# Kernel optimization log

Measured on AMD Instinct MI355X. Metric: run time of the kernel, lower is better.

The kernel has to match this reference:

```python
import jax, jax.numpy as jnp
import numpy as np

WS = 7          # window size
NH = 12         # num heads
DIM = 384
HD = DIM // NH  # head dim = 32
EPS = 1e-5


def _ln(x, g, b):
    m = x.mean(-1, keepdims=True)
    v = ((x - m) ** 2).mean(-1, keepdims=True)
    return (x - m) / jnp.sqrt(v + EPS) * g + b


def _rel_index():
    # exact replica of WindowAttention.__init__ relative_position_index
    coords = np.stack(np.meshgrid(np.arange(WS), np.arange(WS), indexing='ij'))  # (2,ws,ws)
    flat = coords.reshape(2, -1)                                                 # (2,49)
    rel = flat[:, :, None] - flat[:, None, :]                                    # (2,49,49)
    rel = rel.transpose(1, 2, 0).astype(np.int32)
    rel[:, :, 0] += WS - 1
    rel[:, :, 1] += WS - 1
    rel[:, :, 0] *= 2 * WS - 1
    return jnp.asarray(rel.sum(-1))  # (49,49), values in [0, 169)


def setup_inputs() -> dict:
    key = jax.random.key(0)
    ks = jax.random.split(key, 16)
    B, H, W = 16, 56, 56
    L = H * W
    hidden = int(DIM * 4.0)
    p = lambda k, shp: (jax.random.normal(k, shp, jnp.float32) * 0.02)
    return {
        'x': jax.random.normal(ks[0], (B, L, DIM), jnp.float32),
        'kv': jax.random.normal(ks[1], (2, B, NH, WS * WS, HD), jnp.float32),
        'rel_index': _rel_index(),
        'H': H, 'W': W,
        'g1': jnp.ones((DIM,), jnp.float32), 'b1': jnp.zeros((DIM,), jnp.float32),
        'Wqkv': p(ks[2], (DIM, 3 * DIM)), 'bqkv': jnp.zeros((3 * DIM,), jnp.float32),
        'bias_table': p(ks[3], ((2 * WS - 1) ** 2, NH)),
        'Wproj': p(ks[4], (DIM, DIM)), 'bproj': jnp.zeros((DIM,), jnp.float32),
        'g2': jnp.ones((DIM,), jnp.float32), 'b2': jnp.zeros((DIM,), jnp.float32),
        'Wfc1': p(ks[5], (DIM, hidden)), 'bfc1': jnp.zeros((hidden,), jnp.float32),
        'Wfc2': p(ks[6], (hidden, DIM)), 'bfc2': jnp.zeros((DIM,), jnp.float32),
    }


def reference(x, kv, rel_index, H, W, g1, b1, Wqkv, bqkv, bias_table, Wproj, bproj,
              g2, b2, Wfc1, bfc1, Wfc2, bfc2):
    B, L, C = x.shape
    scale = HD ** -0.5
    nWh, nWw = H // WS, W // WS  # H,W divisible by WS -> pad is a no-op; shift_size=0 -> no roll/mask

    h = _ln(x, g1, b1).reshape(B, H, W, C)
    # window_partition -> (B*nW, N, C), N = WS*WS
    hw = h.reshape(B, nWh, WS, nWw, WS, C).transpose(0, 1, 3, 2, 4, 5).reshape(-1, WS * WS, C)
    B_, N, _ = hw.shape

    qkv = (hw @ Wqkv + bqkv).reshape(B_, N, 3, NH, HD).transpose(2, 0, 3, 1, 4)  # (3,B_,nh,N,hd)
    q = qkv[0] * scale
    k, v = kv[0], kv[1]                     # (B, nh, num_kv, hd)
    reps = B_ // k.shape[0]
    k = jnp.repeat(k, reps, axis=0)         # repeat_interleave: each image's windows share its kv
    v = jnp.repeat(v, reps, axis=0)

    attn = jnp.einsum('bhqd,bhkd->bhqk', q, k)                      # (B_,nh,N,N)
    bias = bias_table[rel_index.reshape(-1)].reshape(N, N, NH).transpose(2, 0, 1)
    attn = jax.nn.softmax(attn + bias[None], axis=-1)
    o = jnp.einsum('bhqk,bhkd->bhqd', attn, v)                      # (B_,nh,N,hd)
    o = o.transpose(0, 2, 1, 3).reshape(B_, N, C) @ Wproj + bproj

    # window_reverse -> (B, L, C)
    o = o.reshape(B, nWh, nWw, WS, WS, C).transpose(0, 1, 3, 2, 4, 5).reshape(B, L, C)
    x = x + o
    x = x + (jax.nn.gelu(_ln(x, g2, b2) @ Wfc1 + bfc1, approximate=False) @ Wfc2 + bfc2)
    return x
```

## Files before the change

### kernel.cpp

```cpp
#include <hip/hip_runtime.h>

typedef __attribute__((ext_vector_type(8))) short short8;
typedef __attribute__((ext_vector_type(4))) float floatx4;
typedef unsigned int u32;

#define DIM 384
#define NHEAD 12
#define HDIM 32

__device__ __forceinline__ float bf2f(unsigned int u) {
    union { unsigned int i; float f; } x; x.i = (u & 0xffffu) << 16; return x.f;
}
__device__ __forceinline__ unsigned short f2bf(float f) {
    union { float f; unsigned int i; } x; x.f = f;
    return (unsigned short)((x.i + 0x7fffu + ((x.i >> 16) & 1u)) >> 16);
}

__device__ __forceinline__ int nat2win(int r) {
    int b = r / 3136; int l = r - b * 3136;
    int hh = l / 56, wc = l - hh * 56;
    int wh = hh / 7, nr = hh - wh * 7;
    int ww = wc / 7, nc = wc - ww * 7;
    return ((b << 6) + wh * 8 + ww) * 49 + nr * 7 + nc;
}
__device__ __forceinline__ int win2nat(int r) {
    int w = r / 49; int n = r - w * 49;
    int b = w >> 6; int wi = w & 63;
    int wh = wi >> 3, ww = wi & 7;
    int hh = wh * 7 + n / 7, wc = ww * 7 + n % 7;
    return b * 3136 + hh * 56 + wc;
}

#define GLOAD_LDS16(g, l) \
    __builtin_amdgcn_global_load_lds((const __attribute__((address_space(1))) u32*)(g), \
                                     (__attribute__((address_space(3))) u32*)(l), 16, 0, 0)

__global__ void transpose_kernel(const float* __restrict__ src,
                                 unsigned short* __restrict__ dst,
                                 int K, int N, int ld) {
    int i = blockIdx.x * blockDim.x + threadIdx.x;
    if (i >= K * N) return;
    int n = i / K, k = i - n * K;
    dst[i] = f2bf(src[(size_t)k * ld + n]);
}

__global__ void bias_expand_kernel(const int* __restrict__ rel_index,
                                   const float* __restrict__ bias_table,
                                   float* __restrict__ biasx) {
    int i = blockIdx.x * blockDim.x + threadIdx.x;
    if (i >= NHEAD * 49 * 49) return;
    int h = i / 2401, r = i - h * 2401;
    biasx[i] = bias_table[rel_index[r] * NHEAD + h];
}

__global__ __launch_bounds__(64) void ln_kernel(const float* __restrict__ x,
                                                const float* __restrict__ g,
                                                const float* __restrict__ b,
                                                unsigned short* __restrict__ out,
                                                int windowed) {
    int r = blockIdx.x;
    int lane = threadIdx.x;
    const float* row = x + (size_t)r * DIM;
    float v[6];
    float s = 0.f, ss = 0.f;
#pragma unroll
    for (int j = 0; j < 3; j++) {
        int c = lane + j * 64;
        float2 f = *(const float2*)(row + 2 * c);
        v[2 * j] = f.x; v[2 * j + 1] = f.y;
        s += f.x + f.y; ss += f.x * f.x + f.y * f.y;
    }
#pragma unroll
    for (int m = 1; m < 64; m <<= 1) {
        s += __shfl_xor(s, m);
        ss += __shfl_xor(ss, m);
    }
    float mean = s * (1.f / DIM);
    float var = ss * (1.f / DIM) - mean * mean;
    float rstd = rsqrtf(var + 1e-5f);
    int orow = windowed ? nat2win(r) : r;
    unsigned short* op = out + (size_t)orow * DIM;
#pragma unroll
    for (int j = 0; j < 3; j++) {
        int c = lane + j * 64;
        float2 gg = *(const float2*)(g + 2 * c);
        float2 bb = *(const float2*)(b + 2 * c);
        float o0 = (v[2 * j] - mean) * rstd * gg.x + bb.x;
        float o1 = (v[2 * j + 1] - mean) * rstd * gg.y + bb.y;
        unsigned int w = ((unsigned int)f2bf(o1) << 16) | f2bf(o0);
        *(unsigned int*)(op + 2 * c) = w;
    }
}

__global__ __launch_bounds__(256) void attn_kernel(const unsigned short* __restrict__ q,
                                                   const float* __restrict__ kv,
                                                   const float* __restrict__ biasx,
                                                   unsigned short* __restrict__ o) {
    __shared__ alignas(16) unsigned short Ks[64 * 40];
    __shared__ alignas(16) unsigned short Vt[32 * 72];
    __shared__ float Bi[49 * 52];
    __shared__ alignas(16) unsigned short Ps[4][16 * 72];

    int blk = blockIdx.x;
    int b = blk / 48; int rem = blk - b * 48;
    int h = rem >> 2; int g = rem & 3;
    size_t row_base = (size_t)(b * 64 + g * 16) * 49;

    int t = threadIdx.x;
    int lane = t & 63;
    int wv = t >> 6;
    int lr = lane & 15;
    int lg = lane >> 4;

    const float* kptr = kv + (size_t)(b * NHEAD + h) * 1568;
    for (int idx = t; idx < 392; idx += 256) {
        int row = idx >> 3, seg = idx & 7;
        float4 f = *(const float4*)(kptr + row * 32 + seg * 4);
        ushort4 h4; h4.x = f2bf(f.x); h4.y = f2bf(f.y); h4.z = f2bf(f.z); h4.w = f2bf(f.w);
        *(ushort4*)&Ks[row * 40 + seg * 4] = h4;
    }
    const float* vptr = kv + (size_t)(192 + b * NHEAD + h) * 1568;
    for (int idx = t; idx < 784; idx += 256) {
        int m = idx >> 4, dp = idx & 15;
        float2 f = *(const float2*)(vptr + m * 32 + dp * 2);
        Vt[(2 * dp) * 72 + m]     = f2bf(f.x);
        Vt[(2 * dp + 1) * 72 + m] = f2bf(f.y);
    }
    for (int idx = t; idx < 32 * 23; idx += 256) {
        int d = idx / 23, m = 49 + idx - d * 23;
        Vt[d * 72 + m] = 0;
    }
    const float* bh = biasx + h * 2401;
    for (int idx = t; idx < 2401; idx += 256) {
        int qr = idx / 49, k = idx - qr * 49;
        Bi[qr * 52 + k] = bh[idx];
    }
    __syncthreads();

    short8 bfr[4], vbf[2][2];
#pragma unroll
    for (int ni = 0; ni < 4; ni++)
        bfr[ni] = *(const short8*)&Ks[(ni * 16 + lr) * 40 + lg * 8];
#pragma unroll
    for (int ni = 0; ni < 2; ni++)
#pragma unroll
        for (int ks = 0; ks < 2; ks++)
            vbf[ni][ks] = *(const short8*)&Vt[(ni * 16 + lr) * 72 + ks * 32 + lg * 8];

    const unsigned short* qb = q + row_base * DIM + h * 32 + lg * 8;
    unsigned short* ob = o + row_base * DIM + h * 32;

    short8 af = *(const short8*)(qb + (size_t)(wv * 16 + lr) * DIM);
    for (int tm = wv; tm < 49; tm += 4) {
        short8 af_next;
        if (tm + 4 < 49) af_next = *(const short8*)(qb + (size_t)((tm + 4) * 16 + lr) * DIM);

        floatx4 sfrag[4];
#pragma unroll
        for (int ni = 0; ni < 4; ni++)
            sfrag[ni] = __builtin_amdgcn_mfma_f32_16x16x32_bf16(af, bfr[ni], (floatx4)0.f, 0, 0, 0);

#pragma unroll
        for (int reg = 0; reg < 4; reg++) {
            int r_loc = tm * 16 + lg * 4 + reg;
            int qr = r_loc % 49;
            float mx = -1e30f;
#pragma unroll
            for (int ni = 0; ni < 4; ni++) {
                int k = ni * 16 + lr;
                float s = sfrag[ni][reg];
                if (k < 49) s += Bi[qr * 52 + k];
                else s = -1e30f;
                sfrag[ni][reg] = s;
                mx = fmaxf(mx, s);
            }
#pragma unroll
            for (int j = 1; j < 16; j <<= 1) mx = fmaxf(mx, __shfl_xor(mx, j));
            float sum = 0.f;
#pragma unroll
            for (int ni = 0; ni < 4; ni++) {
                float e = __expf(sfrag[ni][reg] - mx);
                sfrag[ni][reg] = e;
                sum += e;
            }
#pragma unroll
            for (int j = 1; j < 16; j <<= 1) sum += __shfl_xor(sum, j);
            float inv = 1.f / sum;
#pragma unroll
            for (int ni = 0; ni < 4; ni++)
                Ps[wv][(lg * 4 + reg) * 72 + ni * 16 + lr] = f2bf(sfrag[ni][reg] * inv);
        }
        floatx4 ofrag[2] = {(floatx4)0.f, (floatx4)0.f};
#pragma unroll
        for (int ks = 0; ks < 2; ks++) {
            short8 paf = *(const short8*)&Ps[wv][lr * 72 + ks * 32 + lg * 8];
#pragma unroll
            for (int ni = 0; ni < 2; ni++)
                ofrag[ni] = __builtin_amdgcn_mfma_f32_16x16x32_bf16(paf, vbf[ni][ks], ofrag[ni], 0, 0, 0);
        }
#pragma unroll
        for (int reg = 0; reg < 4; reg++) {
            size_t rg = (size_t)(tm * 16 + lg * 4 + reg) * DIM;
#pragma unroll
            for (int ni = 0; ni < 2; ni++)
                ob[rg + ni * 16 + lr] = f2bf(ofrag[ni][reg]);
        }
        af = af_next;
    }
}

template <int DO_GELU, int DO_REMAP, int OUT_BF16>
__global__ __launch_bounds__(256) void gemm_kernel(const unsigned short* __restrict__ A,
                                                   const unsigned short* __restrict__ Bt,
                                                   const float* __restrict__ bias,
                                                   const float* __restrict__ res,
                                                   void* __restrict__ outv,
                                                   int M, int N, int K, float scale) {
    __shared__ alignas(16) unsigned short As[2][128 * 64];
    __shared__ alignas(16) unsigned short Bs[2][128 * 64];
    int m0 = blockIdx.y * 128;
    int n0 = blockIdx.x * 128;
    int t = threadIdx.x;
    int lane = t & 63;
    int wv = t >> 6;
    int wm = (wv >> 1) * 64, wn = (wv & 1) * 64;
    int lr = lane & 15;
    int lq = lane >> 4;

    int rowB = t >> 3;
    int colOff = (((t & 7) ^ ((t >> 3) & 7)) << 3);
    int sw0 = ((lq ^ (lr & 7)) << 3);
    int sw1 = (((4 + lq) ^ (lr & 7)) << 3);

    floatx4 acc[4][4];
#pragma unroll
    for (int i = 0; i < 4; i++)
#pragma unroll
        for (int j = 0; j < 4; j++) acc[i][j] = (floatx4)0.f;

    auto stage = [&](int buf, int kk) {
#pragma unroll
        for (int i = 0; i < 4; i++) {
            int row = i * 32 + rowB;
            GLOAD_LDS16(A + (size_t)(m0 + row) * K + kk + colOff, &As[buf][(i * 256 + t) * 8]);
            GLOAD_LDS16(Bt + (size_t)(n0 + row) * K + kk + colOff, &Bs[buf][(i * 256 + t) * 8]);
        }
    };

    const int nk = K >> 6;
    stage(0, 0);
    stage(1, 64);

    for (int kt = 0; kt < nk; ++kt) {
        int cur = kt & 1;
        if (kt + 1 < nk) asm volatile("s_waitcnt vmcnt(8)" ::: "memory");
        else             asm volatile("s_waitcnt vmcnt(0)" ::: "memory");
        __builtin_amdgcn_s_barrier();
        asm volatile("" ::: "memory");
#pragma unroll
        for (int ksub = 0; ksub < 2; ksub++) {
            int sw = ksub ? sw1 : sw0;
            short8 af[4], bfr[4];
#pragma unroll
            for (int i = 0; i < 4; i++) {
                af[i] = *(const short8*)(&As[cur][(wm + i * 16 + lr) * 64 + sw]);
                bfr[i] = *(const short8*)(&Bs[cur][(wn + i * 16 + lr) * 64 + sw]);
            }
#pragma unroll
            for (int i = 0; i < 4; i++)
#pragma unroll
                for (int j = 0; j < 4; j++)
                    acc[i][j] = __builtin_amdgcn_mfma_f32_16x16x32_bf16(af[i], bfr[j], acc[i][j], 0, 0, 0);
        }
        __builtin_amdgcn_s_barrier();
        asm volatile("" ::: "memory");
        if (kt + 2 < nk) stage(cur, (kt + 2) << 6);
    }

#pragma unroll
    for (int j = 0; j < 4; j++) {
        int gcol = n0 + wn + j * 16 + lr;
        float bv = bias[gcol];
#pragma unroll
        for (int i = 0; i < 4; i++) {
#pragma unroll
            for (int r = 0; r < 4; r++) {
                int grow = m0 + wm + i * 16 + lq * 4 + r;
                float val = acc[i][j][r] + bv;
                if (DO_GELU) val = 0.5f * val * (1.f + erff(val * 0.70710678118654752f));
                val *= scale;
                int orow = DO_REMAP ? win2nat(grow) : grow;
                size_t idx = (size_t)orow * N + gcol;
                if (res) val += res[idx];
                if (OUT_BF16) ((unsigned short*)outv)[idx] = f2bf(val);
                else          ((float*)outv)[idx] = val;
            }
        }
    }
}

extern "C" void kernel_launch(void* const* d_in, const int* in_sizes, int n_in,
                              void* d_out, int out_size, void* d_ws, size_t ws_size,
                              hipStream_t stream) {
    const float* x          = (const float*)d_in[0];
    const float* kv         = (const float*)d_in[1];
    const int*   rel_index  = (const int*)d_in[2];
    const float* g1         = (const float*)d_in[5];
    const float* b1         = (const float*)d_in[6];
    const float* Wqkv       = (const float*)d_in[7];
    const float* bqkv       = (const float*)d_in[8];
    const float* bias_table = (const float*)d_in[9];
    const float* Wproj      = (const float*)d_in[10];
    const float* bproj      = (const float*)d_in[11];
    const float* g2         = (const float*)d_in[12];
    const float* b2         = (const float*)d_in[13];
    const float* Wfc1       = (const float*)d_in[14];
    const float* bfc1       = (const float*)d_in[15];
    const float* Wfc2       = (const float*)d_in[16];
    const float* bfc2       = (const float*)d_in[17];
    float* out = (float*)d_out;

    char* ws = (char*)d_ws;
    unsigned short* wq_t   = (unsigned short*)(ws);
    unsigned short* wp_t   = (unsigned short*)(ws + 294912);
    unsigned short* wfc1_t = (unsigned short*)(ws + 589824);
    unsigned short* wfc2_t = (unsigned short*)(ws + 1769472);
    float*          biasx  = (float*)(ws + 2949120);
    unsigned short* bufA   = (unsigned short*)(ws + 3080192);
    unsigned short* bufB   = (unsigned short*)(ws + 3080192 + 38535168);

    const int M = 50176;
    const float scale = 0.17677669529663687f;
    const int full_mlp = (ws_size >= (size_t)3080192 + 38535168 + 154140672);

    transpose_kernel<<<(384 * 384 + 255) / 256, 256, 0, stream>>>(Wqkv, wq_t, 384, 384, 1152);
    transpose_kernel<<<(384 * 384 + 255) / 256, 256, 0, stream>>>(Wproj, wp_t, 384, 384, 384);
    transpose_kernel<<<(384 * 1536 + 255) / 256, 256, 0, stream>>>(Wfc1, wfc1_t, 384, 1536, 1536);
    transpose_kernel<<<(1536 * 384 + 255) / 256, 256, 0, stream>>>(Wfc2, wfc2_t, 1536, 384, 384);
    bias_expand_kernel<<<(NHEAD * 2401 + 255) / 256, 256, 0, stream>>>(rel_index, bias_table, biasx);

    ln_kernel<<<M, 64, 0, stream>>>(x, g1, b1, bufA, 1);
    gemm_kernel<0, 0, 1><<<dim3(3, 392), 256, 0, stream>>>(bufA, wq_t, bqkv, nullptr, bufB,
                                                           M, 384, 384, scale);
    attn_kernel<<<16 * NHEAD * 4, 256, 0, stream>>>(bufB, kv, biasx, bufA);
    gemm_kernel<0, 1, 0><<<dim3(3, 392), 256, 0, stream>>>(bufA, wp_t, bproj, x, d_out,
                                                           M, 384, 384, 1.f);
    ln_kernel<<<M, 64, 0, stream>>>(out, g2, b2, bufA, 0);

    if (full_mlp) {
        gemm_kernel<1, 0, 1><<<dim3(12, 392), 256, 0, stream>>>(bufA, wfc1_t, bfc1,
                                                                nullptr, bufB, M, 1536, 384, 1.f);
        gemm_kernel<0, 0, 0><<<dim3(3, 392), 256, 0, stream>>>(bufB, wfc2_t, bfc2,
                                                               out, out, M, 384, 1536, 1.f);
    } else {
        for (int c = 0; c < 4; c++) {
            size_t ro = (size_t)c * 12544;
            gemm_kernel<1, 0, 1><<<dim3(12, 98), 256, 0, stream>>>(bufA + ro * 384, wfc1_t, bfc1,
                                                                   nullptr, bufB, 12544, 1536, 384, 1.f);
            gemm_kernel<0, 0, 0><<<dim3(3, 98), 256, 0, stream>>>(bufB, wfc2_t, bfc2,
                                                                  out + ro * 384, out + ro * 384,
                                                                  12544, 384, 1536, 1.f);
        }
    }
}
```

Before: 678.2 us.

## Fuse MLP fc1+GELU+fc2 into one kernel keeping hidden activations on-chip

Replaces the two separate MLP GEMM launches (fc1 with GELU writing a large bf16 hidden buffer, then fc2 reading it back) with a single fused kernel. Each 64-row block computes 128-column hidden chunks with MFMA, applies bias and GELU, stages them in LDS per wave, and accumulates the fc2 output in 24 register accumulators. This removes the global round-trip of the 50176x1536 hidden tensor. In exchange, weights are read directly from global memory without LDS tiling or reuse across waves, and register pressure is high, which may limit occupancy.

```diff
diff --git a/kernel.cpp b/kernel.cpp
--- a/kernel.cpp
+++ b/kernel.cpp
@@ -295,6 +295,80 @@
                 if (OUT_BF16) ((unsigned short*)outv)[idx] = f2bf(val);
                 else          ((float*)outv)[idx] = val;
             }
+        }
+    }
+}
+
+__global__ __launch_bounds__(256, 2) void fused_mlp_kernel(
+    const unsigned short* __restrict__ A,
+    const unsigned short* __restrict__ W1t,
+    const unsigned short* __restrict__ W2t,
+    const float* __restrict__ b1,
+    const float* __restrict__ b2,
+    float* __restrict__ io) {
+    __shared__ alignas(16) unsigned short hl[4][16 * 136];
+
+    int t = threadIdx.x;
+    int lane = t & 63;
+    int wv = t >> 6;
+    int lr = lane & 15;
+    int lg = lane >> 4;
+    int r0 = blockIdx.x * 64 + wv * 16;
+
+    const unsigned short* arow = A + (size_t)(r0 + lr) * 384 + lg * 8;
+    unsigned short* hw = &hl[wv][0];
+
+    floatx4 oacc[24];
+#pragma unroll
+    for (int j = 0; j < 24; j++) oacc[j] = (floatx4)0.f;
+
+    for (int c = 0; c < 12; c++) {
+        __syncthreads();
+
+        floatx4 S[8];
+#pragma unroll
+        for (int n = 0; n < 8; n++) S[n] = (floatx4)0.f;
+        const unsigned short* w1 = W1t + (size_t)(c * 128 + lr) * 384 + lg * 8;
+#pragma unroll
+        for (int k = 0; k < 12; k++) {
+            short8 af = *(const short8*)(arow + k * 32);
+#pragma unroll
+            for (int n = 0; n < 8; n++) {
+                short8 bf = *(const short8*)(w1 + (size_t)(n * 16) * 384 + k * 32);
+                S[n] = __builtin_amdgcn_mfma_f32_16x16x32_bf16(af, bf, S[n], 0, 0, 0);
+            }
+        }
+
+#pragma unroll
+        for (int n = 0; n < 8; n++) {
+            float bb = b1[c * 128 + n * 16 + lr];
+#pragma unroll
+            for (int reg = 0; reg < 4; reg++) {
+                float v = S[n][reg] + bb;
+                v = 0.5f * v * (1.f + erff(v * 0.70710678118654752f));
+                hw[(lg * 4 + reg) * 136 + n * 16 + lr] = f2bf(v);
+            }
+        }
+
+        const unsigned short* w2 = W2t + (size_t)lr * 1536 + c * 128 + lg * 8;
+#pragma unroll
+        for (int k2 = 0; k2 < 4; k2++) {
+            short8 paf = *(const short8*)&hw[lr * 136 + k2 * 32 + lg * 8];
+#pragma unroll
+            for (int n2 = 0; n2 < 24; n2++) {
+                short8 bf2 = *(const short8*)(w2 + (size_t)(n2 * 16) * 1536 + k2 * 32);
+                oacc[n2] = __builtin_amdgcn_mfma_f32_16x16x32_bf16(paf, bf2, oacc[n2], 0, 0, 0);
+            }
+        }
+    }
+
+#pragma unroll
+    for (int n2 = 0; n2 < 24; n2++) {
+        float bb = b2[n2 * 16 + lr];
+#pragma unroll
+        for (int reg = 0; reg < 4; reg++) {
+            size_t idx = (size_t)(r0 + lg * 4 + reg) * 384 + n2 * 16 + lr;
+            io[idx] = io[idx] + oacc[n2][reg] + bb;
         }
     }
 }
@@ -331,7 +405,6 @@
 
     const int M = 50176;
     const float scale = 0.17677669529663687f;
-    const int full_mlp = (ws_size >= (size_t)3080192 + 38535168 + 154140672);
 
     transpose_kernel<<<(384 * 384 + 255) / 256, 256, 0, stream>>>(Wqkv, wq_t, 384, 384, 1152);
     transpose_kernel<<<(384 * 384 + 255) / 256, 256, 0, stream>>>(Wproj, wp_t, 384, 384, 384);
@@ -346,20 +419,7 @@
     gemm_kernel<0, 1, 0><<<dim3(3, 392), 256, 0, stream>>>(bufA, wp_t, bproj, x, d_out,
                                                            M, 384, 384, 1.f);
     ln_kernel<<<M, 64, 0, stream>>>(out, g2, b2, bufA, 0);
-
-    if (full_mlp) {
-        gemm_kernel<1, 0, 1><<<dim3(12, 392), 256, 0, stream>>>(bufA, wfc1_t, bfc1,
-                                                                nullptr, bufB, M, 1536, 384, 1.f);
-        gemm_kernel<0, 0, 0><<<dim3(3, 392), 256, 0, stream>>>(bufB, wfc2_t, bfc2,
-                                                               out, out, M, 384, 1536, 1.f);
-    } else {
-        for (int c = 0; c < 4; c++) {
-            size_t ro = (size_t)c * 12544;
-            gemm_kernel<1, 0, 1><<<dim3(12, 98), 256, 0, stream>>>(bufA + ro * 384, wfc1_t, bfc1,
-                                                                   nullptr, bufB, 12544, 1536, 384, 1.f);
-            gemm_kernel<0, 0, 0><<<dim3(3, 98), 256, 0, stream>>>(bufB, wfc2_t, bfc2,
-                                                                  out + ro * 384, out + ro * 384,
-                                                                  12544, 384, 1536, 1.f);
-        }
-    }
-}
+    fused_mlp_kernel<<<M / 64, 256, 0, stream>>>(bufA, wfc1_t, wfc2_t, bfc1, bfc2, out);
+
+    (void)bufB; (void)ws_size;
+}
```

New measurement: 1.430 ms. 2.11x slower.

## Remap GEMM workgroups across XCDs and stage A through registers

Applied to the files above, without the earlier changes.

Remaps the linear workgroup id so that each XCD gets a contiguous range of output tiles, which is meant to improve L2 locality across the eight XCDs. It also changes the A-operand path from direct global-to-LDS loads to register-staged loads that are prefetched one extra k-step ahead, while B keeps the direct LDS path. The vmcnt waits are restructured to match the new load ordering. This adds register pressure and extra waits in the mainloop, and a wrong vmcnt count could expose stale data.

```diff
diff --git a/kernel.cpp b/kernel.cpp
--- a/kernel.cpp
+++ b/kernel.cpp
@@ -218,8 +218,15 @@
                                                    int M, int N, int K, float scale) {
     __shared__ alignas(16) unsigned short As[2][128 * 64];
     __shared__ alignas(16) unsigned short Bs[2][128 * 64];
-    int m0 = blockIdx.y * 128;
-    int n0 = blockIdx.x * 128;
+
+    int nwg = gridDim.x * gridDim.y;
+    int lid = blockIdx.y * gridDim.x + blockIdx.x;
+    int q8 = nwg >> 3, r8 = nwg & 7;
+    int xcd = lid & 7, pos = lid >> 3;
+    int nlid = (xcd < r8 ? xcd * (q8 + 1) : r8 * (q8 + 1) + (xcd - r8) * q8) + pos;
+    int m0 = (nlid / gridDim.x) * 128;
+    int n0 = (nlid % gridDim.x) * 128;
+
     int t = threadIdx.x;
     int lane = t & 63;
     int wv = t >> 6;
@@ -238,23 +245,45 @@
 #pragma unroll
         for (int j = 0; j < 4; j++) acc[i][j] = (floatx4)0.f;
 
-    auto stage = [&](int buf, int kk) {
-#pragma unroll
-        for (int i = 0; i < 4; i++) {
-            int row = i * 32 + rowB;
-            GLOAD_LDS16(A + (size_t)(m0 + row) * K + kk + colOff, &As[buf][(i * 256 + t) * 8]);
-            GLOAD_LDS16(Bt + (size_t)(n0 + row) * K + kk + colOff, &Bs[buf][(i * 256 + t) * 8]);
-        }
+    short8 ar[4];
+    const unsigned short* Abase = A + (size_t)(m0 + rowB) * K + colOff;
+    const unsigned short* Bbase = Bt + (size_t)(n0 + rowB) * K + colOff;
+    size_t rstep = (size_t)32 * K;
+
+    auto loadA = [&](int kk) {
+#pragma unroll
+        for (int i = 0; i < 4; i++)
+            ar[i] = *(const short8*)(Abase + (size_t)i * rstep + kk);
     };
+    auto writeA = [&](int buf) {
+#pragma unroll
+        for (int i = 0; i < 4; i++)
+            *(short8*)&As[buf][(i * 256 + t) * 8] = ar[i];
+    };
+    auto gloadB = [&](int buf, int kk) {
+#pragma unroll
+        for (int i = 0; i < 4; i++)
+            GLOAD_LDS16(Bbase + (size_t)i * rstep + kk, &Bs[buf][(i * 256 + t) * 8]);
+    };
 
     const int nk = K >> 6;
-    stage(0, 0);
-    stage(1, 64);
+
+    loadA(0);
+    gloadB(0, 0);
+    asm volatile("s_waitcnt vmcnt(4)" ::: "memory");
+    writeA(0);
+    loadA(64);
+    gloadB(1, 64);
+    asm volatile("s_waitcnt vmcnt(4)" ::: "memory");
+    writeA(1);
+    if (nk > 2) loadA(128);
+    asm volatile("s_waitcnt lgkmcnt(0)" ::: "memory");
 
     for (int kt = 0; kt < nk; ++kt) {
         int cur = kt & 1;
-        if (kt + 1 < nk) asm volatile("s_waitcnt vmcnt(8)" ::: "memory");
-        else             asm volatile("s_waitcnt vmcnt(0)" ::: "memory");
+        if (kt + 2 < nk)      asm volatile("s_waitcnt vmcnt(8)" ::: "memory");
+        else if (kt + 1 < nk) asm volatile("s_waitcnt vmcnt(4)" ::: "memory");
+        else                  asm volatile("s_waitcnt vmcnt(0)" ::: "memory");
         __builtin_amdgcn_s_barrier();
         asm volatile("" ::: "memory");
 #pragma unroll
@@ -274,7 +303,13 @@
         }
         __builtin_amdgcn_s_barrier();
         asm volatile("" ::: "memory");
-        if (kt + 2 < nk) stage(cur, (kt + 2) << 6);
+        if (kt + 2 < nk) {
+            gloadB(cur, (kt + 2) << 6);
+            asm volatile("s_waitcnt vmcnt(4)" ::: "memory");
+            writeA(cur);
+            if (kt + 3 < nk) loadA((kt + 3) << 6);
+            asm volatile("s_waitcnt lgkmcnt(0)" ::: "memory");
+        }
     }
 
 #pragma unroll
```

Result: faster. 658.0 us (-3.0%).

## Restructure GEMM to 128x384 tiles with register-resident A fragments

Applied to the files above, without the earlier changes.

The GEMM kernel now uses 512-thread blocks that each compute a 128-row by 384-column strip. Only the weight (B) tile is staged in LDS (double-buffered, 96 KB). A fragments are loaded straight from global memory into registers and prefetched one k-step ahead. The goal is to read each A row once per 384 output columns instead of once per 128, and to cut the number of blocks and LDS traffic for A. The cost is far higher LDS use and register pressure (96 accumulator registers per thread), which limits occupancy, and A loads become uncached strided per-lane global reads.

```diff
diff --git a/kernel.cpp b/kernel.cpp
--- a/kernel.cpp
+++ b/kernel.cpp
@@ -210,87 +210,123 @@
 }
 
 template <int DO_GELU, int DO_REMAP, int OUT_BF16>
-__global__ __launch_bounds__(256) void gemm_kernel(const unsigned short* __restrict__ A,
-                                                   const unsigned short* __restrict__ Bt,
-                                                   const float* __restrict__ bias,
-                                                   const float* __restrict__ res,
-                                                   void* __restrict__ outv,
-                                                   int M, int N, int K, float scale) {
-    __shared__ alignas(16) unsigned short As[2][128 * 64];
-    __shared__ alignas(16) unsigned short Bs[2][128 * 64];
+__global__ __launch_bounds__(512, 3) void gemm_kernel(const unsigned short* __restrict__ A,
+                                                      const unsigned short* __restrict__ Bt,
+                                                      const float* __restrict__ bias,
+                                                      const float* __restrict__ res,
+                                                      void* __restrict__ outv,
+                                                      int Nstride, int K, float scale) {
+    __shared__ alignas(16) unsigned short Bs[2][384 * 64];
+
+    int chunk = blockIdx.x;
     int m0 = blockIdx.y * 128;
-    int n0 = blockIdx.x * 128;
+    const unsigned short* Bc = Bt + (size_t)chunk * 384 * K;
+    int colbase = chunk * 384;
+
     int t = threadIdx.x;
     int lane = t & 63;
     int wv = t >> 6;
-    int wm = (wv >> 1) * 64, wn = (wv & 1) * 64;
+    int wm = (wv >> 1) * 32;
+    int wn2 = (wv & 1) * 192;
     int lr = lane & 15;
     int lq = lane >> 4;
 
-    int rowB = t >> 3;
-    int colOff = (((t & 7) ^ ((t >> 3) & 7)) << 3);
+    int colOffB = (((t & 7) ^ ((t >> 3) & 7)) << 3);
     int sw0 = ((lq ^ (lr & 7)) << 3);
     int sw1 = (((4 + lq) ^ (lr & 7)) << 3);
 
-    floatx4 acc[4][4];
-#pragma unroll
-    for (int i = 0; i < 4; i++)
-#pragma unroll
-        for (int j = 0; j < 4; j++) acc[i][j] = (floatx4)0.f;
-
-    auto stage = [&](int buf, int kk) {
-#pragma unroll
-        for (int i = 0; i < 4; i++) {
-            int row = i * 32 + rowB;
-            GLOAD_LDS16(A + (size_t)(m0 + row) * K + kk + colOff, &As[buf][(i * 256 + t) * 8]);
-            GLOAD_LDS16(Bt + (size_t)(n0 + row) * K + kk + colOff, &Bs[buf][(i * 256 + t) * 8]);
+    floatx4 acc[2][12];
+#pragma unroll
+    for (int m = 0; m < 2; m++)
+#pragma unroll
+        for (int n2 = 0; n2 < 12; n2++) acc[m][n2] = (floatx4)0.f;
+
+    const unsigned short* Arow0 = A + (size_t)(m0 + wm + lr) * K + lq * 8;
+    const unsigned short* Arow1 = A + (size_t)(m0 + wm + 16 + lr) * K + lq * 8;
+
+    auto gloadB = [&](int buf, int kk) {
+#pragma unroll
+        for (int i = 0; i < 6; i++) {
+            int slot = i * 512 + t;
+            int row = slot >> 3;
+            GLOAD_LDS16(Bc + (size_t)row * K + kk + colOffB, &Bs[buf][slot * 8]);
         }
     };
 
     const int nk = K >> 6;
-    stage(0, 0);
-    stage(1, 64);
-
-    for (int kt = 0; kt < nk; ++kt) {
-        int cur = kt & 1;
-        if (kt + 1 < nk) asm volatile("s_waitcnt vmcnt(8)" ::: "memory");
-        else             asm volatile("s_waitcnt vmcnt(0)" ::: "memory");
-        __builtin_amdgcn_s_barrier();
-        asm volatile("" ::: "memory");
-#pragma unroll
-        for (int ksub = 0; ksub < 2; ksub++) {
-            int sw = ksub ? sw1 : sw0;
-            short8 af[4], bfr[4];
-#pragma unroll
-            for (int i = 0; i < 4; i++) {
-                af[i] = *(const short8*)(&As[cur][(wm + i * 16 + lr) * 64 + sw]);
-                bfr[i] = *(const short8*)(&Bs[cur][(wn + i * 16 + lr) * 64 + sw]);
+
+    short8 aX00, aX01, aX10, aX11, aY00, aY01, aY10, aY11;
+
+    gloadB(0, 0);
+    aX00 = *(const short8*)(Arow0);
+    aX01 = *(const short8*)(Arow0 + 32);
+    aX10 = *(const short8*)(Arow1);
+    aX11 = *(const short8*)(Arow1 + 32);
+    gloadB(1, 64);
+
+    auto compute = [&](int buf, const short8& a00, const short8& a01,
+                       const short8& a10, const short8& a11) {
+#pragma unroll
+        for (int n2 = 0; n2 < 12; n2++) {
+            int r = wn2 + n2 * 16 + lr;
+            short8 bf0 = *(const short8*)&Bs[buf][r * 64 + sw0];
+            short8 bf1 = *(const short8*)&Bs[buf][r * 64 + sw1];
+            acc[0][n2] = __builtin_amdgcn_mfma_f32_16x16x32_bf16(a00, bf0, acc[0][n2], 0, 0, 0);
+            acc[1][n2] = __builtin_amdgcn_mfma_f32_16x16x32_bf16(a10, bf0, acc[1][n2], 0, 0, 0);
+            acc[0][n2] = __builtin_amdgcn_mfma_f32_16x16x32_bf16(a01, bf1, acc[0][n2], 0, 0, 0);
+            acc[1][n2] = __builtin_amdgcn_mfma_f32_16x16x32_bf16(a11, bf1, acc[1][n2], 0, 0, 0);
+        }
+    };
+
+    for (int kt = 0; kt < nk; kt += 2) {
+        {
+            int kk1 = (kt + 1) << 6;
+            aY00 = *(const short8*)(Arow0 + kk1);
+            aY01 = *(const short8*)(Arow0 + kk1 + 32);
+            aY10 = *(const short8*)(Arow1 + kk1);
+            aY11 = *(const short8*)(Arow1 + kk1 + 32);
+            asm volatile("s_waitcnt vmcnt(10)" ::: "memory");
+            __builtin_amdgcn_s_barrier();
+            asm volatile("" ::: "memory");
+            compute(0, aX00, aX01, aX10, aX11);
+            __builtin_amdgcn_s_barrier();
+            asm volatile("" ::: "memory");
+            if (kt + 2 < nk) gloadB(0, (kt + 2) << 6);
+        }
+        {
+            if (kt + 2 < nk) {
+                int kk2 = (kt + 2) << 6;
+                aX00 = *(const short8*)(Arow0 + kk2);
+                aX01 = *(const short8*)(Arow0 + kk2 + 32);
+                aX10 = *(const short8*)(Arow1 + kk2);
+                aX11 = *(const short8*)(Arow1 + kk2 + 32);
+                asm volatile("s_waitcnt vmcnt(10)" ::: "memory");
+            } else {
+                asm volatile("s_waitcnt vmcnt(0)" ::: "memory");
             }
-#pragma unroll
-            for (int i = 0; i < 4; i++)
-#pragma unroll
-                for (int j = 0; j < 4; j++)
-                    acc[i][j] = __builtin_amdgcn_mfma_f32_16x16x32_bf16(af[i], bfr[j], acc[i][j], 0, 0, 0);
-        }
-        __builtin_amdgcn_s_barrier();
-        asm volatile("" ::: "memory");
-        if (kt + 2 < nk) stage(cur, (kt + 2) << 6);
-    }
-
-#pragma unroll
-    for (int j = 0; j < 4; j++) {
-        int gcol = n0 + wn + j * 16 + lr;
+            __builtin_amdgcn_s_barrier();
+            asm volatile("" ::: "memory");
+            compute(1, aY00, aY01, aY10, aY11);
+            __builtin_amdgcn_s_barrier();
+            asm volatile("" ::: "memory");
+            if (kt + 3 < nk) gloadB(1, (kt + 3) << 6);
+        }
+    }
+
+#pragma unroll
+    for (int n2 = 0; n2 < 12; n2++) {
+        int gcol = colbase + wn2 + n2 * 16 + lr;
         float bv = bias[gcol];
 #pragma unroll
-        for (int i = 0; i < 4; i++) {
+        for (int m = 0; m < 2; m++) {
 #pragma unroll
             for (int r = 0; r < 4; r++) {
-                int grow = m0 + wm + i * 16 + lq * 4 + r;
-                float val = acc[i][j][r] + bv;
+                int grow = m0 + wm + m * 16 + lq * 4 + r;
+                float val = acc[m][n2][r] + bv;
                 if (DO_GELU) val = 0.5f * val * (1.f + erff(val * 0.70710678118654752f));
                 val *= scale;
                 int orow = DO_REMAP ? win2nat(grow) : grow;
-                size_t idx = (size_t)orow * N + gcol;
+                size_t idx = (size_t)orow * Nstride + gcol;
                 if (res) val += res[idx];
                 if (OUT_BF16) ((unsigned short*)outv)[idx] = f2bf(val);
                 else          ((float*)outv)[idx] = val;
@@ -340,26 +376,26 @@
     bias_expand_kernel<<<(NHEAD * 2401 + 255) / 256, 256, 0, stream>>>(rel_index, bias_table, biasx);
 
     ln_kernel<<<M, 64, 0, stream>>>(x, g1, b1, bufA, 1);
-    gemm_kernel<0, 0, 1><<<dim3(3, 392), 256, 0, stream>>>(bufA, wq_t, bqkv, nullptr, bufB,
-                                                           M, 384, 384, scale);
+    gemm_kernel<0, 0, 1><<<dim3(1, M / 128), 512, 0, stream>>>(bufA, wq_t, bqkv, nullptr, bufB,
+                                                               384, 384, scale);
     attn_kernel<<<16 * NHEAD * 4, 256, 0, stream>>>(bufB, kv, biasx, bufA);
-    gemm_kernel<0, 1, 0><<<dim3(3, 392), 256, 0, stream>>>(bufA, wp_t, bproj, x, d_out,
-                                                           M, 384, 384, 1.f);
+    gemm_kernel<0, 1, 0><<<dim3(1, M / 128), 512, 0, stream>>>(bufA, wp_t, bproj, x, d_out,
+                                                               384, 384, 1.f);
     ln_kernel<<<M, 64, 0, stream>>>(out, g2, b2, bufA, 0);
 
     if (full_mlp) {
-        gemm_kernel<1, 0, 1><<<dim3(12, 392), 256, 0, stream>>>(bufA, wfc1_t, bfc1,
-                                                                nullptr, bufB, M, 1536, 384, 1.f);
-        gemm_kernel<0, 0, 0><<<dim3(3, 392), 256, 0, stream>>>(bufB, wfc2_t, bfc2,
-                                                               out, out, M, 384, 1536, 1.f);
+        gemm_kernel<1, 0, 1><<<dim3(4, M / 128), 512, 0, stream>>>(bufA, wfc1_t, bfc1,
+                                                                   nullptr, bufB, 1536, 384, 1.f);
+        gemm_kernel<0, 0, 0><<<dim3(1, M / 128), 512, 0, stream>>>(bufB, wfc2_t, bfc2,
+                                                                   out, out, 384, 1536, 1.f);
     } else {
         for (int c = 0; c < 4; c++) {
             size_t ro = (size_t)c * 12544;
-            gemm_kernel<1, 0, 1><<<dim3(12, 98), 256, 0, stream>>>(bufA + ro * 384, wfc1_t, bfc1,
-                                                                   nullptr, bufB, 12544, 1536, 384, 1.f);
-            gemm_kernel<0, 0, 0><<<dim3(3, 98), 256, 0, stream>>>(bufB, wfc2_t, bfc2,
+            gemm_kernel<1, 0, 1><<<dim3(4, 98), 512, 0, stream>>>(bufA + ro * 384, wfc1_t, bfc1,
+                                                                  nullptr, bufB, 1536, 384, 1.f);
+            gemm_kernel<0, 0, 0><<<dim3(1, 98), 512, 0, stream>>>(bufB, wfc2_t, bfc2,
                                                                   out + ro * 384, out + ro * 384,
-                                                                  12544, 384, 1536, 1.f);
-        }
-    }
-}
+                                                                  384, 1536, 1.f);
+        }
+    }
+}
```

Result: slower. 721.2 us (+6.3%).
